# Kernel optimization log

Measured on AMD Instinct MI355X. Metric: run time of the kernel, lower is better.

The kernel has to match this reference:

```python
import jax, jax.numpy as jnp
import numpy as np

MAX_DEG = 10  # PyG MFConv default max_degree


def mfconv(x, edge_index, W, b, Wr):
    """Degree-bucketed graph conv (PyG MFConv).
    x: [N, F_in]; edge_index: [2, E]; W, Wr: [MAX_DEG+1, F_in, F_out]; b: [MAX_DEG+1, F_out].
    out_i = lins[deg_i](sum_{j in N(i)} x_j) + root_lins[deg_i](x_i)
    """
    N = x.shape[0]
    src, dst = edge_index[0], edge_index[1]
    # sum-aggregate neighbor features (gather + scatter-add)
    h = jax.ops.segment_sum(x[src], dst, num_segments=N)  # [N, F_in]
    # in-degree per node, clamped to MAX_DEG
    deg = jax.ops.segment_sum(jnp.ones_like(dst, dtype=jnp.int32), dst, num_segments=N)
    deg = jnp.clip(deg, 0, MAX_DEG)  # [N]
    # compute all degree-bucket outputs, then select per node ([N, D+1, F_out] is small)
    out_all = jnp.einsum('nf,dfo->ndo', h, W) + b[None] + jnp.einsum('nf,dfo->ndo', x, Wr)
    return jnp.take_along_axis(out_all, deg[:, None, None], axis=1)[:, 0]  # [N, F_out]


def setup_inputs() -> dict:
    key = jax.random.key(0)
    ks = jax.random.split(key, 8)
    N, E = 100000, 1600000
    F_in, F_hid, F_out = 128, 32, 64
    D = MAX_DEG + 1
    x = jax.random.normal(ks[0], (N, F_in), dtype=jnp.float32)
    edge_index = jax.random.randint(ks[1], (2, E), 0, N, dtype=jnp.int64)
    s1 = 1.0 / np.sqrt(F_in)
    s2 = 1.0 / np.sqrt(F_hid)
    W1 = jax.random.uniform(ks[2], (D, F_in, F_hid), jnp.float32, -s1, s1)
    b1 = jax.random.uniform(ks[3], (D, F_hid), jnp.float32, -s1, s1)
    Wr1 = jax.random.uniform(ks[4], (D, F_in, F_hid), jnp.float32, -s1, s1)
    W2 = jax.random.uniform(ks[5], (D, F_hid, F_out), jnp.float32, -s2, s2)
    b2 = jax.random.uniform(ks[6], (D, F_out), jnp.float32, -s2, s2)
    Wr2 = jax.random.uniform(ks[7], (D, F_hid, F_out), jnp.float32, -s2, s2)
    return {"x": x, "edge_index": edge_index, "W1": W1, "b1": b1, "Wr1": Wr1,
            "W2": W2, "b2": b2, "Wr2": Wr2}


def reference(x, edge_index, W1, b1, Wr1, W2, b2, Wr2):
    h = mfconv(x, edge_index, W1, b1, Wr1)
    h = jax.nn.relu(h)
    return mfconv(h, edge_index, W2, b2, Wr2)
```

## Files before the change

kernel.cpp:

```cpp
#include <hip/hip_runtime.h>

#define FIN 128
#define FHID 32
#define FOUT 64
#define MAXDEG 10
#define BSH 8
#define ACHUNK 4096
#define XPAD 136
#define YPAD 40
#define SRCBITS 20

typedef __attribute__((ext_vector_type(8))) short short8;
typedef __attribute__((ext_vector_type(4))) float f32x4;


__device__ __forceinline__ float bf2f(unsigned short u) {
    union { unsigned int i; float f; } c; c.i = ((unsigned int)u) << 16; return c.f;
}
__device__ __forceinline__ unsigned short f2bf(float f) {
    union { float f; unsigned int i; } c; c.f = f;
    unsigned int r = c.i + 0x7FFF + ((c.i >> 16) & 1);
    return (unsigned short)(r >> 16);
}
__device__ __forceinline__ float bflo(unsigned int w) { return bf2f((unsigned short)(w & 0xffff)); }
__device__ __forceinline__ float bfhi(unsigned int w) { return bf2f((unsigned short)(w >> 16)); }
__device__ __forceinline__ unsigned int pk2(float lo, float hi) {
    return (unsigned int)f2bf(lo) | ((unsigned int)f2bf(hi) << 16);
}


__global__ __launch_bounds__(256) void k_bhistp(const int* __restrict__ ei, int E, int N,
                                                int* __restrict__ bcnt,
                                                const float* __restrict__ W1,
                                                const float* __restrict__ Wr1,
                                                const float* __restrict__ W2,
                                                const float* __restrict__ Wr2,
                                                unsigned short* __restrict__ wcat1,
                                                unsigned short* __restrict__ wcat2) {
    __shared__ int hist[1024];
    int K = ((N + 255) >> BSH);
    int t = threadIdx.x;
    long long cb = (long long)blockIdx.x * ACHUNK;
    for (int i = t; i < K; i += 256) hist[i] = 0;
    __syncthreads();
#pragma unroll
    for (int i = 0; i < 16; ++i) {
        long long e = cb + t + (long long)i * 256;
        if (e < E) {
            int ss = ei[e];
            int dd = ei[E + e];
            if ((unsigned)ss < (unsigned)N && (unsigned)dd < (unsigned)N)
                atomicAdd(&hist[dd >> BSH], 1);
        }
    }
    __syncthreads();
    for (int i = t; i < K; i += 256) {
        int h = hist[i];
        if (h) atomicAdd(&bcnt[i], h);
    }
    if (blockIdx.x == 0) {
        const float* W1b  = W1  + (size_t)MAXDEG * FIN * FHID;
        const float* Wr1b = Wr1 + (size_t)MAXDEG * FIN * FHID;
        const float* W2b  = W2  + (size_t)MAXDEG * FHID * FOUT;
        const float* Wr2b = Wr2 + (size_t)MAXDEG * FHID * FOUT;
        for (int i = 0; i < 32; ++i) {
            int idx = i * 256 + t;
            int n = idx >> 7, k = idx & 127;
            float v = (n < 32) ? W1b[k * FHID + n] : Wr1b[k * FHID + (n - 32)];
            wcat1[idx] = f2bf(v);
        }
        for (int i = 0; i < 16; ++i) {
            int idx = i * 256 + t;
            int n = idx >> 5, k = idx & 31;
            float v = (n < 64) ? W2b[k * FOUT + n] : Wr2b[k * FOUT + (n - 64)];
            wcat2[idx] = f2bf(v);
        }
    }
}

__global__ __launch_bounds__(1024) void k_scanb(const int* __restrict__ bcnt, int K,
                                                int* __restrict__ bstart,
                                                int* __restrict__ gcur) {
    __shared__ int tmp[1024];
    int t = threadIdx.x;
    int v = (t < K) ? bcnt[t] : 0;
    tmp[t] = v;
    __syncthreads();
    for (int off = 1; off < 1024; off <<= 1) {
        int a = (t >= off) ? tmp[t - off] : 0;
        __syncthreads();
        tmp[t] += a;
        __syncthreads();
    }
    if (t < K) { int s = tmp[t] - v; bstart[t] = s; gcur[t] = s; }
}

__global__ __launch_bounds__(256) void k_passA(const int* __restrict__ ei, int E, int N,
                                               int* __restrict__ gcur,
                                               unsigned int* __restrict__ pairs) {
    __shared__ int hist[1024];
    __shared__ int base[1024];
    int K = ((N + 255) >> BSH);
    int t = threadIdx.x;
    long long cb = (long long)blockIdx.x * ACHUNK;
    for (int i = t; i < K; i += 256) hist[i] = 0;
    __syncthreads();
    int sv[16], dv[16];
#pragma unroll
    for (int i = 0; i < 16; ++i) {
        sv[i] = -1; dv[i] = 0;
        long long e = cb + t + (long long)i * 256;
        if (e < E) {
            int ss = ei[e];
            int dd = ei[E + e];
            if ((unsigned)ss < (unsigned)N && (unsigned)dd < (unsigned)N) {
                sv[i] = ss; dv[i] = dd;
            }
        }
    }
#pragma unroll
    for (int i = 0; i < 16; ++i)
        if (sv[i] >= 0) atomicAdd(&hist[dv[i] >> BSH], 1);
    __syncthreads();
    for (int i = t; i < K; i += 256) {
        int h = hist[i];
        base[i] = h ? atomicAdd(&gcur[i], h) : 0;
    }
    __syncthreads();
    for (int i = t; i < K; i += 256) hist[i] = 0;
    __syncthreads();
#pragma unroll
    for (int i = 0; i < 16; ++i) {
        if (sv[i] >= 0) {
            int b = dv[i] >> BSH;
            int off = atomicAdd(&hist[b], 1);
            pairs[base[b] + off] = (unsigned int)sv[i] | ((unsigned int)(dv[i] & 255) << SRCBITS);
        }
    }
}

__global__ __launch_bounds__(256) void k_passB2(const unsigned int* __restrict__ pairs,
                                                const int* __restrict__ bstart,
                                                const int* __restrict__ gcur,
                                                int* __restrict__ deg,
                                                int* __restrict__ cursor,
                                                int* __restrict__ adj,
                                                int* __restrict__ nflag,
                                                int* __restrict__ flist, int N) {
    __shared__ int cnt[256];
    __shared__ int scn[256];
    __shared__ int cur[256];
    __shared__ int fids[256];
    __shared__ int fcnt, fbase;
    int b = blockIdx.x;
    int lo = b << BSH;
    int t = threadIdx.x;
    int nvalid = min(256, N - lo);
    cnt[t] = 0;
    if (t == 0) fcnt = 0;
    int pstart = bstart[b];
    int pend = gcur[b];
    __syncthreads();
    for (int i = pstart + t; i < pend; i += 256)
        atomicAdd(&cnt[pairs[i] >> SRCBITS], 1);
    __syncthreads();
    int v = cnt[t];
    scn[t] = v;
    __syncthreads();
    for (int off = 1; off < 256; off <<= 1) {
        int a = (t >= off) ? scn[t - off] : 0;
        __syncthreads();
        scn[t] += a;
        __syncthreads();
    }
    int rowstart = pstart + scn[t] - v;
    cur[t] = rowstart;
    if (t < nvalid) {
        deg[lo + t] = v;
        cursor[lo + t] = rowstart + v;
        if (v < MAXDEG) { int p = atomicAdd(&fcnt, 1); fids[p] = lo + t; }
    }
    __syncthreads();
    if (t == 0 && fcnt > 0) fbase = atomicAdd(nflag, fcnt);
    __syncthreads();
    if (t < fcnt) flist[fbase + t] = fids[t];
    for (int i = pstart + t; i < pend; i += 256) {
        unsigned int pr = pairs[i];
        int pos = atomicAdd(&cur[pr >> SRCBITS], 1);
        adj[pos] = (int)(pr & ((1u << SRCBITS) - 1));
    }
}

__global__ __launch_bounds__(256) void k_pre1m(const float* __restrict__ x,
                                               const unsigned short* __restrict__ wcat1,
                                               const float* __restrict__ b1,
                                               unsigned short* __restrict__ z10,
                                               unsigned short* __restrict__ r1, int N) {
    __shared__ __align__(16) unsigned short xt[64 * XPAD];
    __shared__ __align__(16) unsigned short wt[64 * XPAD];
    int t = threadIdx.x;
    int row0 = blockIdx.x * 64;
    {
        const uint4* src = (const uint4*)wcat1;
#pragma unroll
        for (int i = 0; i < 4; ++i) {
            int idx = i * 256 + t;
            uint4 v = src[idx];
            int n = idx >> 4;
            int k = (idx & 15) * 8;
            *(uint4*)(wt + n * XPAD + k) = v;
        }
    }
    {
        int r = t >> 2;
        int c0 = (t & 3) * 32;
        int cr = min(row0 + r, N - 1);
        const float4* xs = (const float4*)(x + (size_t)cr * FIN + c0);
        unsigned short* dst = xt + r * XPAD + c0;
#pragma unroll
        for (int i = 0; i < 8; ++i) {
            float4 v = xs[i];
            ushort4 b;
            b.x = f2bf(v.x); b.y = f2bf(v.y); b.z = f2bf(v.z); b.w = f2bf(v.w);
            *(ushort4*)(dst + i * 4) = b;
        }
    }
    __syncthreads();
    int w = t >> 6, lane = t & 63;
    int m = lane & 15, quad = lane >> 4;
    const unsigned short* arow = xt + (w * 16 + m) * XPAD + quad * 8;
    short8 af[4];
#pragma unroll
    for (int kt = 0; kt < 4; ++kt) af[kt] = *(const short8*)(arow + kt * 32);
    f32x4 acc[4];
#pragma unroll
    for (int ct = 0; ct < 4; ++ct) acc[ct] = (f32x4){0.f, 0.f, 0.f, 0.f};
#pragma unroll
    for (int ct = 0; ct < 4; ++ct) {
        const unsigned short* brow = wt + (ct * 16 + m) * XPAD + quad * 8;
#pragma unroll
        for (int kt = 0; kt < 4; ++kt) {
            short8 bfr = *(const short8*)(brow + kt * 32);
            acc[ct] = __builtin_amdgcn_mfma_f32_16x16x32_bf16(af[kt], bfr, acc[ct], 0, 0, 0);
        }
    }
    int rbase = row0 + w * 16 + quad * 4;
#pragma unroll
    for (int ct = 0; ct < 4; ++ct) {
        float bias = (ct >= 2) ? b1[MAXDEG * FHID + (ct - 2) * 16 + m] : 0.f;
#pragma unroll
        for (int rg = 0; rg < 4; ++rg) {
            int n = rbase + rg;
            if (n < N) {
                float v = acc[ct][rg];
                if (ct < 2) z10[(size_t)n * FHID + ct * 16 + m] = f2bf(v);
                else        r1[(size_t)n * FHID + (ct - 2) * 16 + m] = f2bf(v + bias);
            }
        }
    }
}

__device__ __forceinline__ void gather16(const unsigned short* __restrict__ rows,
                                         const int* __restrict__ adj,
                                         int e0, int e1, int cnt, int lane,
                                         float& a0, float& a1) {
    int e = lane >> 4, f2 = lane & 15;
    int sidx = adj[min(e0 + lane, e1 - 1)];
    const unsigned short* rb = rows + f2 * 2;
    int nfull = cnt >> 4;
    for (int c = 0; c < nfull; ++c) {
        int i0 = c * 16 + e;
        int s0 = __shfl(sidx, i0);
        int s1 = __shfl(sidx, i0 + 4);
        int s2 = __shfl(sidx, i0 + 8);
        int s3 = __shfl(sidx, i0 + 12);
        unsigned int w0 = *(const unsigned int*)(rb + (size_t)s0 * FHID);
        unsigned int w1 = *(const unsigned int*)(rb + (size_t)s1 * FHID);
        unsigned int w2 = *(const unsigned int*)(rb + (size_t)s2 * FHID);
        unsigned int w3 = *(const unsigned int*)(rb + (size_t)s3 * FHID);
        a0 += bflo(w0); a1 += bfhi(w0);
        a0 += bflo(w1); a1 += bfhi(w1);
        a0 += bflo(w2); a1 += bfhi(w2);
        a0 += bflo(w3); a1 += bfhi(w3);
    }
    if (cnt & 15) {
        int i0 = nfull * 16 + e;
        int i1 = i0 + 4, i2 = i0 + 8, i3 = i0 + 12;
        int s0 = __shfl(sidx, min(i0, cnt - 1));
        int s1 = __shfl(sidx, min(i1, cnt - 1));
        int s2 = __shfl(sidx, min(i2, cnt - 1));
        int s3 = __shfl(sidx, min(i3, cnt - 1));
        unsigned int w0 = *(const unsigned int*)(rb + (size_t)s0 * FHID);
        unsigned int w1 = *(const unsigned int*)(rb + (size_t)s1 * FHID);
        unsigned int w2 = *(const unsigned int*)(rb + (size_t)s2 * FHID);
        unsigned int w3 = *(const unsigned int*)(rb + (size_t)s3 * FHID);
        float c0 = (i0 < cnt) ? 1.f : 0.f;
        float c1 = (i1 < cnt) ? 1.f : 0.f;
        float c2 = (i2 < cnt) ? 1.f : 0.f;
        float c3 = (i3 < cnt) ? 1.f : 0.f;
        a0 = fmaf(c0, bflo(w0), a0); a1 = fmaf(c0, bfhi(w0), a1);
        a0 = fmaf(c1, bflo(w1), a0); a1 = fmaf(c1, bfhi(w1), a1);
        a0 = fmaf(c2, bflo(w2), a0); a1 = fmaf(c2, bfhi(w2), a1);
        a0 = fmaf(c3, bflo(w3), a0); a1 = fmaf(c3, bfhi(w3), a1);
    }
    for (int k = e0 + 64 + e; k < e1; k += 4) {
        int s = adj[k];
        unsigned int w = *(const unsigned int*)(rb + (size_t)s * FHID);
        a0 += bflo(w); a1 += bfhi(w);
    }
}

__global__ __launch_bounds__(256) void k_layer1x(const unsigned short* __restrict__ z10,
                                                 const unsigned short* __restrict__ r1,
                                                 const int* __restrict__ deg,
                                                 const int* __restrict__ cursor,
                                                 const int* __restrict__ adj,
                                                 const float* __restrict__ x,
                                                 const float* __restrict__ W1,
                                                 const float* __restrict__ b1,
                                                 const float* __restrict__ Wr1,
                                                 const int* __restrict__ nflag,
                                                 const int* __restrict__ flist,
                                                 unsigned short* __restrict__ out1,
                                                 int N, int nbFast) {
    int t = threadIdx.x;
    int lane = t & 63;
    if ((int)blockIdx.x < nbFast) {
        int n = blockIdx.x * 4 + (t >> 6);
        if (n >= N) return;
        int dg = deg[n];
        if (dg < MAXDEG) return;
        int e1 = cursor[n];
        int e0 = e1 - dg;
        float a0 = 0.f, a1 = 0.f;
        gather16(z10, adj, e0, e1, min(dg, 64), lane, a0, a1);
        a0 += __shfl_xor(a0, 16); a1 += __shfl_xor(a1, 16);
        a0 += __shfl_xor(a0, 32); a1 += __shfl_xor(a1, 32);
        if (lane < 16) {
            unsigned int rv = *(const unsigned int*)(r1 + (size_t)n * FHID + lane * 2);
            unsigned int w = pk2(fmaxf(a0 + bflo(rv), 0.f), fmaxf(a1 + bfhi(rv), 0.f));
            *(unsigned int*)(out1 + (size_t)n * FHID + lane * 2) = w;
        }
    } else {
        int wid = ((blockIdx.x - nbFast) * 256 + t) >> 6;
        int nw = (gridDim.x - nbFast) * 4;
        int u = lane >> 5, o = lane & 31;
        int fcnt = *nflag;
        for (int i = wid; i < fcnt; i += nw) {
            int n = flist[i];
            int d = deg[n];
            const float* Wr = Wr1 + (size_t)d * (FIN * FHID) + o;
            const float4* xr = (const float4*)(x + (size_t)n * FIN);
            float racc = 0.f;
            for (int c = u * 16; c < u * 16 + 16; ++c) {
                float4 xv = xr[c];
                racc += xv.x * Wr[(c * 4 + 0) * FHID] + xv.y * Wr[(c * 4 + 1) * FHID]
                      + xv.z * Wr[(c * 4 + 2) * FHID] + xv.w * Wr[(c * 4 + 3) * FHID];
            }
            racc += __shfl_xor(racc, 32);
            int e1 = cursor[n];
            int e0 = e1 - d;
            float2 h = make_float2(0.f, 0.f);
            for (int k = e0; k < e1; ++k) {
                int s = adj[k];
                float2 v = *(const float2*)(x + (size_t)s * FIN + lane * 2);
                h.x += v.x; h.y += v.y;
            }
            const float* Wp = W1 + (size_t)d * (FIN * FHID) + o;
            float acc = 0.f;
            for (int f = u * 64; f < u * 64 + 64; ++f) {
                float hf = __shfl((f & 1) ? h.y : h.x, f >> 1);
                acc += hf * Wp[f * FHID];
            }
            acc += __shfl_xor(acc, 32);
            if (lane < 32) {
                float rv = racc + b1[d * FHID + o];
                out1[(size_t)n * FHID + o] = f2bf(fmaxf(acc + rv, 0.f));
            }
        }
    }
}

__global__ __launch_bounds__(256) void k_layer2g(const unsigned short* __restrict__ y,
                                                 const int* __restrict__ deg,
                                                 const int* __restrict__ cursor,
                                                 const int* __restrict__ adj,
                                                 float* __restrict__ g, int N) {
    int wave = (int)(((long long)blockIdx.x * 256 + threadIdx.x) >> 6);
    if (wave >= N) return;
    int n = wave;
    int lane = threadIdx.x & 63;
    int dg = deg[n];
    float a0 = 0.f, a1 = 0.f;
    if (dg > 0) {
        int e1 = cursor[n];
        int e0 = e1 - dg;
        gather16(y, adj, e0, e1, min(dg, 64), lane, a0, a1);
        a0 += __shfl_xor(a0, 16); a1 += __shfl_xor(a1, 16);
        a0 += __shfl_xor(a0, 32); a1 += __shfl_xor(a1, 32);
    }
    if (lane < 16) {
        *(float2*)(g + (size_t)n * FHID + lane * 2) = make_float2(a0, a1);
    }
}

__global__ __launch_bounds__(256) void k_post2x(const float* __restrict__ g,
                                                const unsigned short* __restrict__ y,
                                                const unsigned short* __restrict__ wcat2,
                                                const float* __restrict__ b2,
                                                const int* __restrict__ deg,
                                                const int* __restrict__ cursor,
                                                const int* __restrict__ adj,
                                                const float* __restrict__ W2full,
                                                const float* __restrict__ Wr2full,
                                                const int* __restrict__ nflag,
                                                const int* __restrict__ flist,
                                                float* __restrict__ out,
                                                int N, int nbFast) {
    int t = threadIdx.x;
    if ((int)blockIdx.x < nbFast) {
        __shared__ __align__(16) unsigned short gt[64 * YPAD];
        __shared__ __align__(16) unsigned short yt[64 * YPAD];
        __shared__ __align__(16) unsigned short wt[128 * YPAD];
        __shared__ unsigned char flg[64];
        int row0 = blockIdx.x * 64;
        {
            const uint4* src = (const uint4*)wcat2;
#pragma unroll
            for (int i = 0; i < 2; ++i) {
                int idx = i * 256 + t;
                uint4 v = src[idx];
                int nn = idx >> 2;
                int k = (idx & 3) * 8;
                *(uint4*)(wt + nn * YPAD + k) = v;
            }
        }
        if (t < 64) {
            int rn = row0 + t;
            flg[t] = (rn < N) ? (unsigned char)(deg[rn] < MAXDEG) : (unsigned char)1;
        }
        {
            int r = t >> 2, c0 = (t & 3) * 8;
            int rn = min(row0 + r, N - 1);
            const float4* gs = (const float4*)(g + (size_t)rn * FHID + c0);
            float4 v0 = gs[0], v1 = gs[1];
            ushort4 p0, p1;
            p0.x = f2bf(v0.x); p0.y = f2bf(v0.y); p0.z = f2bf(v0.z); p0.w = f2bf(v0.w);
            p1.x = f2bf(v1.x); p1.y = f2bf(v1.y); p1.z = f2bf(v1.z); p1.w = f2bf(v1.w);
            *(ushort4*)(gt + r * YPAD + c0) = p0;
            *(ushort4*)(gt + r * YPAD + c0 + 4) = p1;
            uint4 vy = *(const uint4*)(y + (size_t)rn * FHID + c0);
            *(uint4*)(yt + r * YPAD + c0) = vy;
        }
        __syncthreads();
        int w = t >> 6, lane = t & 63;
        int m = lane & 15, quad = lane >> 4;
        short8 ag = *(const short8*)(gt + (w * 16 + m) * YPAD + quad * 8);
        short8 ay = *(const short8*)(yt + (w * 16 + m) * YPAD + quad * 8);
        int rbase = w * 16 + quad * 4;
#pragma unroll
        for (int ct = 0; ct < 4; ++ct) {
            short8 bw = *(const short8*)(wt + (ct * 16 + m) * YPAD + quad * 8);
            short8 br = *(const short8*)(wt + ((64 + ct * 16) + m) * YPAD + quad * 8);
            f32x4 acc = (f32x4){0.f, 0.f, 0.f, 0.f};
            acc = __builtin_amdgcn_mfma_f32_16x16x32_bf16(ag, bw, acc, 0, 0, 0);
            acc = __builtin_amdgcn_mfma_f32_16x16x32_bf16(ay, br, acc, 0, 0, 0);
            int o = ct * 16 + m;
            float bias = b2[MAXDEG * FOUT + o];
#pragma unroll
            for (int rg = 0; rg < 4; ++rg) {
                int rl = rbase + rg;
                int nn = row0 + rl;
                if (nn < N && !flg[rl]) out[(size_t)nn * FOUT + o] = acc[rg] + bias;
            }
        }
    } else {
        int wid = ((blockIdx.x - nbFast) * 256 + t) >> 6;
        int nw = (gridDim.x - nbFast) * 4;
        int lane = t & 63;
        int fcnt = *nflag;
        for (int i = wid; i < fcnt; i += nw) {
            int n = flist[i];
            int d = deg[n];
            float a0 = 0.f, a1 = 0.f;
            if (d > 0) {
                int e1 = cursor[n];
                gather16(y, adj, e1 - d, e1, d, lane, a0, a1);
                a0 += __shfl_xor(a0, 16); a1 += __shfl_xor(a1, 16);
                a0 += __shfl_xor(a0, 32); a1 += __shfl_xor(a1, 32);
            }
            const float* W2p  = W2full  + (size_t)d * (FHID * FOUT) + lane;
            const float* Wr2p = Wr2full + (size_t)d * (FHID * FOUT) + lane;
            unsigned int yw = *(const unsigned int*)(y + (size_t)n * FHID + (lane & 15) * 2);
            float acc = b2[d * FOUT + lane];
#pragma unroll
            for (int q = 0; q < 16; ++q) {
                float g0 = __shfl(a0, q);
                float g1 = __shfl(a1, q);
                unsigned int yq = __shfl(yw, q);
                acc += g0 * W2p[(2 * q) * FOUT] + g1 * W2p[(2 * q + 1) * FOUT]
                     + bflo(yq) * Wr2p[(2 * q) * FOUT] + bfhi(yq) * Wr2p[(2 * q + 1) * FOUT];
            }
            out[(size_t)n * FOUT + lane] = acc;
        }
    }
}

extern "C" void kernel_launch(void* const* d_in, const int* in_sizes, int n_in,
                              void* d_out, int out_size, void* d_ws, size_t ws_size,
                              hipStream_t stream) {
    const float* x   = (const float*)d_in[0];
    const int*   ei  = (const int*)d_in[1];
    const float* W1  = (const float*)d_in[2];
    const float* b1  = (const float*)d_in[3];
    const float* Wr1 = (const float*)d_in[4];
    const float* W2  = (const float*)d_in[5];
    const float* b2  = (const float*)d_in[6];
    const float* Wr2 = (const float*)d_in[7];

    int N = in_sizes[0] / FIN;
    int E = in_sizes[1] / 2;
    int K  = (N + 255) >> BSH;

    char* ws = (char*)d_ws;
    size_t off = 0;
    auto alloc = [&](size_t bytes) {
        void* ptr = ws + off;
        off += (bytes + 511) / 512 * 512;
        return ptr;
    };
    int* deg              = (int*)alloc((size_t)N * sizeof(int));
    int* cursor           = (int*)alloc((size_t)N * sizeof(int));
    int* bcnt             = (int*)alloc((size_t)(K + 1) * sizeof(int));
    int* nflag            = bcnt + K;
    int* bstart           = (int*)alloc((size_t)K * sizeof(int));
    int* gcur             = (int*)alloc((size_t)K * sizeof(int));
    int* flist            = (int*)alloc((size_t)N * sizeof(int));
    int* adj              = (int*)alloc((size_t)E * sizeof(int));
    unsigned short* z10   = (unsigned short*)alloc((size_t)N * FHID * 2);
    unsigned short* r1    = (unsigned short*)alloc((size_t)N * FHID * 2);
    unsigned short* out1  = (unsigned short*)alloc((size_t)N * FHID * 2);
    size_t pairsB = (size_t)E * sizeof(unsigned int);
    size_t gB     = (size_t)N * FHID * sizeof(float);
    void* shared_region   = alloc(pairsB > gB ? pairsB : gB);
    float* g              = (float*)shared_region;
    unsigned int* pairs   = (unsigned int*)shared_region;
    unsigned short* wcat1 = (unsigned short*)alloc(64 * 128 * 2);
    unsigned short* wcat2 = (unsigned short*)alloc(128 * 32 * 2);

    float* out = (float*)d_out;

    (void)hipMemsetAsync(bcnt, 0, (size_t)(K + 1) * sizeof(int), stream);

    int nwgA = (E + ACHUNK - 1) / ACHUNK;
    k_bhistp<<<nwgA, 256, 0, stream>>>(ei, E, N, bcnt, W1, Wr1, W2, Wr2, wcat1, wcat2);
    k_scanb<<<1, 1024, 0, stream>>>(bcnt, K, bstart, gcur);
    k_passA<<<nwgA, 256, 0, stream>>>(ei, E, N, gcur, pairs);
    k_passB2<<<K, 256, 0, stream>>>(pairs, bstart, gcur, deg, cursor, adj, nflag, flist, N);

    int nb64 = (N + 63) / 64;
    int nb_node = (N + 3) / 4;
    const int FIXB = 512;

    k_pre1m<<<nb64, 256, 0, stream>>>(x, wcat1, b1, z10, r1, N);
    k_layer1x<<<nb_node + FIXB, 256, 0, stream>>>(z10, r1, deg, cursor, adj,
                                                  x, W1, b1, Wr1, nflag, flist, out1,
                                                  N, nb_node);
    k_layer2g<<<nb_node, 256, 0, stream>>>(out1, deg, cursor, adj, g, N);
    k_post2x<<<nb64 + FIXB, 256, 0, stream>>>(g, out1, wcat2, b2, deg, cursor, adj,
                                              W2, Wr2, nflag, flist, out, N, nb64);
}
```

Measured before the change: 287.5 us.

## Process four nodes per wavefront in neighbor-gather kernels

The gather kernels for layer 1 and layer 2 now assign four nodes to each 64-lane wavefront instead of one. A new gather16x4 routine interleaves the edge loads of all four nodes and picks each node's sum with lane selects. The average degree is about 16, so a one-node wave left most lanes idle; this raises memory-level parallelism and lane use, at the cost of more registers and divergence when the four degrees differ.

```diff
diff --git a/kernel.cpp b/kernel.cpp
--- a/kernel.cpp
+++ b/kernel.cpp
@@ -310,6 +310,65 @@
     }
 }
 
+__device__ __forceinline__ void gather16x4(const unsigned short* __restrict__ rows,
+                                           const int* __restrict__ adj,
+                                           const int* e0, const int* e1, const int* cnt,
+                                           int lane, float* a0, float* a1) {
+    int e2 = lane >> 4, f2 = lane & 15;
+    const unsigned short* rb = rows + f2 * 2;
+    int cm1[4], sidx[4];
+    int maxc = 0;
+#pragma unroll
+    for (int i = 0; i < 4; ++i) {
+        cm1[i] = max(cnt[i] - 1, 0);
+        sidx[i] = adj[e0[i] + min(lane, cm1[i])];
+        maxc = max(maxc, cnt[i]);
+    }
+    int nch = (maxc + 15) >> 4;
+    for (int c = 0; c < nch; ++c) {
+        int i0 = c * 16 + e2;
+        int i1 = i0 + 4, i2 = i0 + 8, i3 = i0 + 12;
+#pragma unroll
+        for (int i = 0; i < 4; ++i) {
+            int s0 = __shfl(sidx[i], min(i0, cm1[i]));
+            int s1 = __shfl(sidx[i], min(i1, cm1[i]));
+            int s2 = __shfl(sidx[i], min(i2, cm1[i]));
+            int s3 = __shfl(sidx[i], min(i3, cm1[i]));
+            unsigned int w0 = *(const unsigned int*)(rb + (size_t)s0 * FHID);
+            unsigned int w1 = *(const unsigned int*)(rb + (size_t)s1 * FHID);
+            unsigned int w2 = *(const unsigned int*)(rb + (size_t)s2 * FHID);
+            unsigned int w3 = *(const unsigned int*)(rb + (size_t)s3 * FHID);
+            float c0 = (i0 < cnt[i]) ? 1.f : 0.f;
+            float c1 = (i1 < cnt[i]) ? 1.f : 0.f;
+            float c2 = (i2 < cnt[i]) ? 1.f : 0.f;
+            float c3 = (i3 < cnt[i]) ? 1.f : 0.f;
+            a0[i] = fmaf(c0, bflo(w0), a0[i]); a1[i] = fmaf(c0, bfhi(w0), a1[i]);
+            a0[i] = fmaf(c1, bflo(w1), a0[i]); a1[i] = fmaf(c1, bfhi(w1), a1[i]);
+            a0[i] = fmaf(c2, bflo(w2), a0[i]); a1[i] = fmaf(c2, bfhi(w2), a1[i]);
+            a0[i] = fmaf(c3, bflo(w3), a0[i]); a1[i] = fmaf(c3, bfhi(w3), a1[i]);
+        }
+    }
+#pragma unroll
+    for (int i = 0; i < 4; ++i) {
+        for (int k = e0[i] + 64 + e2; k < e1[i]; k += 4) {
+            int s = adj[k];
+            unsigned int w = *(const unsigned int*)(rb + (size_t)s * FHID);
+            a0[i] += bflo(w); a1[i] += bfhi(w);
+        }
+    }
+}
+
+__device__ __forceinline__ float sel4(const float* a, int g) {
+    float lo = (g & 1) ? a[1] : a[0];
+    float hi = (g & 1) ? a[3] : a[2];
+    return (g & 2) ? hi : lo;
+}
+__device__ __forceinline__ int sel4i(const int* a, int g) {
+    int lo = (g & 1) ? a[1] : a[0];
+    int hi = (g & 1) ? a[3] : a[2];
+    return (g & 2) ? hi : lo;
+}
+
 __global__ __launch_bounds__(256) void k_layer1x(const unsigned short* __restrict__ z10,
                                                  const unsigned short* __restrict__ r1,
                                                  const int* __restrict__ deg,
@@ -326,20 +385,38 @@
     int t = threadIdx.x;
     int lane = t & 63;
     if ((int)blockIdx.x < nbFast) {
-        int n = blockIdx.x * 4 + (t >> 6);
-        if (n >= N) return;
-        int dg = deg[n];
-        if (dg < MAXDEG) return;
-        int e1 = cursor[n];
-        int e0 = e1 - dg;
-        float a0 = 0.f, a1 = 0.f;
-        gather16(z10, adj, e0, e1, min(dg, 64), lane, a0, a1);
-        a0 += __shfl_xor(a0, 16); a1 += __shfl_xor(a1, 16);
-        a0 += __shfl_xor(a0, 32); a1 += __shfl_xor(a1, 32);
-        if (lane < 16) {
-            unsigned int rv = *(const unsigned int*)(r1 + (size_t)n * FHID + lane * 2);
-            unsigned int w = pk2(fmaxf(a0 + bflo(rv), 0.f), fmaxf(a1 + bfhi(rv), 0.f));
-            *(unsigned int*)(out1 + (size_t)n * FHID + lane * 2) = w;
+        int nb = blockIdx.x * 16 + (t >> 6) * 4;
+        if (nb >= N) return;
+        int nl = min(nb + (lane & 3), N - 1);
+        int dl = deg[nl];
+        int cl = cursor[nl];
+        int dg[4], e1v[4], e0v[4], cntv[4];
+#pragma unroll
+        for (int i = 0; i < 4; ++i) {
+            dg[i] = __shfl(dl, i);
+            e1v[i] = __shfl(cl, i);
+            bool ok = (nb + i < N) && (dg[i] >= MAXDEG);
+            cntv[i] = ok ? min(dg[i], 64) : 0;
+            e0v[i] = e1v[i] - dg[i];
+            if (!ok) e1v[i] = e0v[i];
+        }
+        if ((cntv[0] | cntv[1] | cntv[2] | cntv[3]) == 0) return;
+        float a0[4] = {0.f, 0.f, 0.f, 0.f};
+        float a1[4] = {0.f, 0.f, 0.f, 0.f};
+        gather16x4(z10, adj, e0v, e1v, cntv, lane, a0, a1);
+#pragma unroll
+        for (int i = 0; i < 4; ++i) {
+            a0[i] += __shfl_xor(a0[i], 16); a1[i] += __shfl_xor(a1[i], 16);
+            a0[i] += __shfl_xor(a0[i], 32); a1[i] += __shfl_xor(a1[i], 32);
+        }
+        int g = lane >> 4, f2 = lane & 15;
+        int cg = sel4i(cntv, g);
+        if (cg > 0) {
+            int ng = nb + g;
+            float v0 = sel4(a0, g), v1 = sel4(a1, g);
+            unsigned int rv = *(const unsigned int*)(r1 + (size_t)ng * FHID + f2 * 2);
+            unsigned int w = pk2(fmaxf(v0 + bflo(rv), 0.f), fmaxf(v1 + bfhi(rv), 0.f));
+            *(unsigned int*)(out1 + (size_t)ng * FHID + f2 * 2) = w;
         }
     } else {
         int wid = ((blockIdx.x - nbFast) * 256 + t) >> 6;
@@ -386,21 +463,36 @@
                                                  const int* __restrict__ cursor,
                                                  const int* __restrict__ adj,
                                                  float* __restrict__ g, int N) {
-    int wave = (int)(((long long)blockIdx.x * 256 + threadIdx.x) >> 6);
-    if (wave >= N) return;
-    int n = wave;
-    int lane = threadIdx.x & 63;
-    int dg = deg[n];
-    float a0 = 0.f, a1 = 0.f;
-    if (dg > 0) {
-        int e1 = cursor[n];
-        int e0 = e1 - dg;
-        gather16(y, adj, e0, e1, min(dg, 64), lane, a0, a1);
-        a0 += __shfl_xor(a0, 16); a1 += __shfl_xor(a1, 16);
-        a0 += __shfl_xor(a0, 32); a1 += __shfl_xor(a1, 32);
-    }
-    if (lane < 16) {
-        *(float2*)(g + (size_t)n * FHID + lane * 2) = make_float2(a0, a1);
+    int t = threadIdx.x;
+    int lane = t & 63;
+    int nb = blockIdx.x * 16 + (t >> 6) * 4;
+    if (nb >= N) return;
+    int nl = min(nb + (lane & 3), N - 1);
+    int dl = deg[nl];
+    int cl = cursor[nl];
+    int dg[4], e1v[4], e0v[4], cntv[4];
+#pragma unroll
+    for (int i = 0; i < 4; ++i) {
+        dg[i] = __shfl(dl, i);
+        e1v[i] = __shfl(cl, i);
+        bool ok = (nb + i < N);
+        cntv[i] = ok ? min(dg[i], 64) : 0;
+        e0v[i] = e1v[i] - dg[i];
+        if (!ok) e1v[i] = e0v[i];
+    }
+    float a0[4] = {0.f, 0.f, 0.f, 0.f};
+    float a1[4] = {0.f, 0.f, 0.f, 0.f};
+    gather16x4(y, adj, e0v, e1v, cntv, lane, a0, a1);
+#pragma unroll
+    for (int i = 0; i < 4; ++i) {
+        a0[i] += __shfl_xor(a0[i], 16); a1[i] += __shfl_xor(a1[i], 16);
+        a0[i] += __shfl_xor(a0[i], 32); a1[i] += __shfl_xor(a1[i], 32);
+    }
+    int gg = lane >> 4, f2 = lane & 15;
+    int ng = nb + gg;
+    if (ng < N) {
+        float v0 = sel4(a0, gg), v1 = sel4(a1, gg);
+        *(float2*)(g + (size_t)ng * FHID + f2 * 2) = make_float2(v0, v1);
     }
 }
 
@@ -559,14 +651,14 @@
     k_passB2<<<K, 256, 0, stream>>>(pairs, bstart, gcur, deg, cursor, adj, nflag, flist, N);
 
     int nb64 = (N + 63) / 64;
-    int nb_node = (N + 3) / 4;
+    int nb_quad = (N + 15) / 16;
     const int FIXB = 512;
 
     k_pre1m<<<nb64, 256, 0, stream>>>(x, wcat1, b1, z10, r1, N);
-    k_layer1x<<<nb_node + FIXB, 256, 0, stream>>>(z10, r1, deg, cursor, adj,
+    k_layer1x<<<nb_quad + FIXB, 256, 0, stream>>>(z10, r1, deg, cursor, adj,
                                                   x, W1, b1, Wr1, nflag, flist, out1,
-                                                  N, nb_node);
-    k_layer2g<<<nb_node, 256, 0, stream>>>(out1, deg, cursor, adj, g, N);
+                                                  N, nb_quad);
+    k_layer2g<<<nb_quad, 256, 0, stream>>>(out1, deg, cursor, adj, g, N);
     k_post2x<<<nb64 + FIXB, 256, 0, stream>>>(g, out1, wcat2, b2, deg, cursor, adj,
                                               W2, Wr2, nflag, flist, out, N, nb64);
 }
```

Measured after the change: 286.5 us. About the same (-0.3%).
